# Kernel optimization log

Measured on AMD Instinct MI355X. Metric: run time of the kernel, lower is better.

The kernel has to match this reference:

```python
import jax, jax.numpy as jnp
import numpy as np

N_NODES = 100000
N_EDGES = 1600000
IN_DIM = 128
OUT_DIM = 64


def setup_inputs() -> dict:
    key = jax.random.key(0)
    k1, k2, k3, k4 = jax.random.split(key, 4)
    h = jax.random.normal(k1, (N_NODES, IN_DIM), dtype=jnp.float32)
    W = jax.random.normal(k2, (OUT_DIM, IN_DIM), dtype=jnp.float32) * (1.0 / np.sqrt(IN_DIM))
    a_w = jax.random.normal(k3, (1, 2 * OUT_DIM), dtype=jnp.float32) * (1.0 / np.sqrt(2 * OUT_DIM))
    edge_index = jax.random.randint(k4, (2, N_EDGES), 0, N_NODES, dtype=jnp.int64 if jax.config.jax_enable_x64 else jnp.int32)
    return {"h": h, "W": W, "a_w": a_w, "edge_index": edge_index}


def reference(h, W, a_w, edge_index):
    # Wh: [N, out_dim]  (Linear without bias: x @ W.T)
    Wh = h @ W.T
    src, dst = edge_index[0], edge_index[1]
    # per-edge concat [Wh[src], Wh[dst]] -> [E, 2*out_dim]
    e = jnp.concatenate([Wh[src], Wh[dst]], axis=-1)
    # attention logits: [E]
    alpha = jax.nn.leaky_relu(e @ a_w.T, negative_slope=0.2)[:, 0]
    # global-max-stabilized exp (matches the torch code exactly)
    alpha_exp = jnp.exp(alpha - jnp.max(alpha))
    # segment softmax denominator over destination nodes: [N]
    alpha_sum = jax.ops.segment_sum(alpha_exp, dst, num_segments=N_NODES)
    alpha_norm = alpha_exp / (alpha_sum[dst] + 1e-9)
    # weighted scatter-add aggregation: [N, out_dim]
    out = jax.ops.segment_sum(alpha_norm[:, None] * Wh[src], dst, num_segments=N_NODES)
    return (jax.nn.elu(out), alpha_norm)
```

## Files before the change

### kernel.cpp

```cpp
#include <hip/hip_runtime.h>
#include <math.h>

#define N_NODES 100000
#define N_EDGES 1600000
#define IN_DIM 128
#define OUT_DIM 64

#define BSHIFT 7
#define BSIZE  (1 << BSHIFT)
#define NB     ((N_NODES + BSIZE - 1) >> BSHIFT)
#define EDGES_PER_BLK 4096
#define NBLK   ((N_EDGES + EDGES_PER_BLK - 1) / EDGES_PER_BLK)
#define SCANA_LEN (NB * NBLK)
#define SCANA_ITEMS 1024
#define SCANA_NB ((SCANA_LEN + SCANA_ITEMS - 1) / SCANA_ITEMS)
#define REC_CAP 3072

typedef short short8 __attribute__((ext_vector_type(8)));
typedef float f32x4 __attribute__((ext_vector_type(4)));
typedef float f32x2 __attribute__((ext_vector_type(2)));

__device__ __forceinline__ unsigned short f2bf(float x) {
    unsigned int u = __float_as_uint(x);
    return (unsigned short)((u + 0x7FFFu + ((u >> 16) & 1u)) >> 16);
}
__device__ __forceinline__ short8 pack_bf16x8(float4 p, float4 q) {
    short8 r;
    r[0] = (short)f2bf(p.x); r[1] = (short)f2bf(p.y);
    r[2] = (short)f2bf(p.z); r[3] = (short)f2bf(p.w);
    r[4] = (short)f2bf(q.x); r[5] = (short)f2bf(q.y);
    r[6] = (short)f2bf(q.z); r[7] = (short)f2bf(q.w);
    return r;
}
__device__ __forceinline__ void pk_fma(f32x2& d, f32x2 a, f32x2 b) {
    asm("v_pk_fma_f32 %0, %1, %2, %0" : "+v"(d) : "v"(a), "v"(b));
}

__global__ __launch_bounds__(256) void k_histA(const int* __restrict__ dst,
                                               int* __restrict__ hist_t,
                                               const float* __restrict__ W,
                                               const float* __restrict__ a_w,
                                               float* __restrict__ w1,
                                               float* __restrict__ w2) {
    __shared__ int lhist[NB];
    const int tid = threadIdx.x;
    const int blk = blockIdx.x;
    if (blk == 0 && tid < IN_DIM) {
        float r1 = 0.f, r2 = 0.f;
        #pragma unroll 8
        for (int dd = 0; dd < OUT_DIM; ++dd) {
            float wv = W[dd * IN_DIM + tid];
            r1 = fmaf(a_w[dd], wv, r1);
            r2 = fmaf(a_w[OUT_DIM + dd], wv, r2);
        }
        w1[tid] = r1; w2[tid] = r2;
    }
    for (int i = tid; i < NB; i += 256) lhist[i] = 0;
    __syncthreads();
    const int e0 = blk * EDGES_PER_BLK;
    #pragma unroll
    for (int j = 0; j < 4; ++j) {
        int e = e0 + (j * 256 + tid) * 4;
        if (e >= N_EDGES) continue;
        int4 d4 = *(const int4*)(dst + e);
        atomicAdd(&lhist[d4.x >> BSHIFT], 1);
        atomicAdd(&lhist[d4.y >> BSHIFT], 1);
        atomicAdd(&lhist[d4.z >> BSHIFT], 1);
        atomicAdd(&lhist[d4.w >> BSHIFT], 1);
    }
    __syncthreads();
    for (int i = tid; i < NB; i += 256) hist_t[i * NBLK + blk] = lhist[i];
}

__global__ __launch_bounds__(256) void k_wh(const float* __restrict__ h,
                                            const float* __restrict__ W,
                                            const float* __restrict__ w1,
                                            const float* __restrict__ w2,
                                            unsigned short* __restrict__ Wh16,
                                            float* __restrict__ s1,
                                            float* __restrict__ s2) {
    const int tid = threadIdx.x;
    const int wv = tid >> 6;
    const int l  = tid & 63;
    const int g  = l >> 4;
    const int lm = l & 15;
    const int node0 = blockIdx.x * 64 + wv * 16;
    const int row = node0 + lm;
    const int rowc = (row < N_NODES) ? row : (N_NODES - 1);
    const float* hrow = h + (size_t)rowc * IN_DIM;

    short8 afrag[4];
    float sp1 = 0.f, sp2 = 0.f;
    #pragma unroll
    for (int kt = 0; kt < 4; ++kt) {
        const int k0 = kt * 32 + g * 8;
        float4 p = *(const float4*)(hrow + k0);
        float4 q = *(const float4*)(hrow + k0 + 4);
        float4 u1 = *(const float4*)(w1 + k0);
        float4 v1 = *(const float4*)(w1 + k0 + 4);
        float4 u2 = *(const float4*)(w2 + k0);
        float4 v2 = *(const float4*)(w2 + k0 + 4);
        sp1 += p.x*u1.x + p.y*u1.y + p.z*u1.z + p.w*u1.w
             + q.x*v1.x + q.y*v1.y + q.z*v1.z + q.w*v1.w;
        sp2 += p.x*u2.x + p.y*u2.y + p.z*u2.z + p.w*u2.w
             + q.x*v2.x + q.y*v2.y + q.z*v2.z + q.w*v2.w;
        afrag[kt] = pack_bf16x8(p, q);
    }
    sp1 += __shfl_xor(sp1, 16, 64); sp1 += __shfl_xor(sp1, 32, 64);
    sp2 += __shfl_xor(sp2, 16, 64); sp2 += __shfl_xor(sp2, 32, 64);
    if (l < 16 && row < N_NODES) { s1[row] = sp1; s2[row] = sp2; }

    f32x4 acc[4] = {f32x4{0,0,0,0}, f32x4{0,0,0,0}, f32x4{0,0,0,0}, f32x4{0,0,0,0}};
    #pragma unroll
    for (int nt = 0; nt < 4; ++nt) {
        #pragma unroll
        for (int kt = 0; kt < 4; ++kt) {
            const float* wr = W + (size_t)(nt * 16 + lm) * IN_DIM + kt * 32 + g * 8;
            float4 p = *(const float4*)wr;
            float4 q = *(const float4*)(wr + 4);
            short8 bfrag = pack_bf16x8(p, q);
            acc[nt] = __builtin_amdgcn_mfma_f32_16x16x32_bf16(afrag[kt], bfrag, acc[nt], 0, 0, 0);
        }
    }
    #pragma unroll
    for (int nt = 0; nt < 4; ++nt) {
        #pragma unroll
        for (int r = 0; r < 4; ++r) {
            int nodo = node0 + g * 4 + r;
            if (nodo < N_NODES)
                Wh16[(size_t)nodo * OUT_DIM + nt * 16 + lm] = f2bf(acc[nt][r]);
        }
    }
}

__global__ __launch_bounds__(256) void k_scanA_part(const int* __restrict__ in,
                                                    int* __restrict__ bsum) {
    __shared__ int wsum[4];
    const int tid = threadIdx.x;
    const int base = blockIdx.x * SCANA_ITEMS + tid * 4;
    int s = 0;
    #pragma unroll
    for (int j = 0; j < 4; ++j) {
        int i = base + j;
        if (i < SCANA_LEN) s += in[i];
    }
    #pragma unroll
    for (int off = 32; off > 0; off >>= 1) s += __shfl_xor(s, off, 64);
    if ((tid & 63) == 0) wsum[tid >> 6] = s;
    __syncthreads();
    if (tid == 0) bsum[blockIdx.x] = wsum[0] + wsum[1] + wsum[2] + wsum[3];
}

__global__ __launch_bounds__(512) void k_scanA_mid(int* __restrict__ bsum) {
    __shared__ int s[512];
    const int tid = threadIdx.x;
    s[tid] = (tid < SCANA_NB) ? bsum[tid] : 0;
    __syncthreads();
    #pragma unroll
    for (int off = 1; off < 512; off <<= 1) {
        int u = (tid >= off) ? s[tid - off] : 0;
        __syncthreads();
        s[tid] += u;
        __syncthreads();
    }
    if (tid < SCANA_NB) bsum[tid] = (tid > 0) ? s[tid - 1] : 0;
}

__global__ __launch_bounds__(256) void k_scanA_final(const int* __restrict__ in,
                                                     const int* __restrict__ bsum,
                                                     int* __restrict__ outscan) {
    __shared__ int wtot[4];
    const int tid = threadIdx.x;
    const int lane = tid & 63;
    const int wid = tid >> 6;
    const int base = blockIdx.x * SCANA_ITEMS + tid * 4;
    int c[4];
    #pragma unroll
    for (int j = 0; j < 4; ++j)
        c[j] = (base + j < SCANA_LEN) ? in[base + j] : 0;
    int tot = c[0] + c[1] + c[2] + c[3];
    int inc = tot;
    #pragma unroll
    for (int off = 1; off < 64; off <<= 1) {
        int u = __shfl_up(inc, off, 64);
        if (lane >= off) inc += u;
    }
    if (lane == 63) wtot[wid] = inc;
    __syncthreads();
    int wbase = 0;
    #pragma unroll
    for (int w = 0; w < 4; ++w) wbase += (w < wid) ? wtot[w] : 0;
    int run = bsum[blockIdx.x] + wbase + (inc - tot);
    #pragma unroll
    for (int j = 0; j < 4; ++j) {
        int i = base + j;
        if (i < SCANA_LEN) { outscan[i] = run; run += c[j]; }
    }
}

__global__ __launch_bounds__(256) void k_binA(const int* __restrict__ ei,
                                              const float* __restrict__ s1,
                                              const float* __restrict__ s2,
                                              const int* __restrict__ flat_scan,
                                              int2* __restrict__ brec,
                                              float* __restrict__ ae_orig) {
    __shared__ int lbase[NB];
    __shared__ int lcur[NB];
    const int tid = threadIdx.x;
    const int blk = blockIdx.x;
    for (int i = tid; i < NB; i += 256) { lbase[i] = flat_scan[i * NBLK + blk]; lcur[i] = 0; }
    __syncthreads();
    const int e0 = blk * EDGES_PER_BLK;
    #pragma unroll
    for (int j = 0; j < 4; ++j) {
        int e = e0 + (j * 256 + tid) * 4;
        if (e >= N_EDGES) continue;
        int4 s4 = *(const int4*)(ei + e);
        int4 d4 = *(const int4*)(ei + N_EDGES + e);
        float4 aev;
        #pragma unroll
        for (int q = 0; q < 4; ++q) {
            int src = ((const int*)&s4)[q];
            int dst = ((const int*)&d4)[q];
            float a = s1[src] + s2[dst];
            a = (a > 0.f) ? a : 0.2f * a;
            float ae = expf(a);
            ((float*)&aev)[q] = ae;
            int b = dst >> BSHIFT;
            int r = atomicAdd(&lcur[b], 1);
            brec[lbase[b] + r] = make_int2(src | ((dst & (BSIZE - 1)) << 17),
                                           __float_as_int(ae));
        }
        *(float4*)(ae_orig + e) = aev;
    }
}

__global__ __launch_bounds__(256) void k_fineagg(const int2* __restrict__ brec,
                                                 const int* __restrict__ flat_scan,
                                                 const unsigned short* __restrict__ Wh16,
                                                 float* __restrict__ out,
                                                 float* __restrict__ inv_tab) {
    __shared__ int2 lsorted[REC_CAP];
    __shared__ int lhist[BSIZE];
    __shared__ int lofs[BSIZE + 1];
    __shared__ int lcur[BSIZE];
    __shared__ float linv[BSIZE];
    const int tid = threadIdx.x;
    const int lane = tid & 63;
    const int wid = tid >> 6;
    const int b = blockIdx.x;
    const int base = flat_scan[b * NBLK];
    const int endp = (b + 1 < NB) ? flat_scan[(b + 1) * NBLK] : N_EDGES;
    const int cnt = endp - base;
    if (tid < BSIZE) lhist[tid] = 0;
    __syncthreads();
    for (int i = tid; i < cnt; i += 256)
        atomicAdd(&lhist[(unsigned)brec[base + i].x >> 17], 1);
    __syncthreads();
    if (wid == 0) {
        int c0 = lhist[2 * lane], c1 = lhist[2 * lane + 1];
        int s = c0 + c1;
        int inc = s;
        #pragma unroll
        for (int off = 1; off < 64; off <<= 1) {
            int u = __shfl_up(inc, off, 64);
            if (lane >= off) inc += u;
        }
        int ex = inc - s;
        lofs[2 * lane] = ex; lofs[2 * lane + 1] = ex + c0;
        lcur[2 * lane] = ex; lcur[2 * lane + 1] = ex + c0;
        if (lane == 63) lofs[BSIZE] = inc;
    }
    __syncthreads();
    for (int i = tid; i < cnt; i += 256) {
        int2 rec = brec[base + i];
        int dstl = (unsigned)rec.x >> 17;
        int pos = atomicAdd(&lcur[dstl], 1);
        lsorted[pos] = make_int2(rec.x & 0x1FFFF, rec.y);
    }
    __syncthreads();
    const int g = lane >> 3;
    const int o = lane & 7;
    const int dst0 = b << BSHIFT;
    for (int j = 0; j < 32; ++j) {
        const int bin = wid * 32 + j;
        const int node = dst0 + bin;
        if (node >= N_NODES) break;
        const int beg = lofs[bin];
        const int end2 = lofs[bin + 1];
        f32x2 acc2[4] = {f32x2{0,0}, f32x2{0,0}, f32x2{0,0}, f32x2{0,0}};
        float S = 0.f;
        int i = beg;
        for (; i + 16 <= end2; i += 16) {
            int2 pA = lsorted[i + g];
            int2 pB = lsorted[i + 8 + g];
            const int4 rA = *(const int4*)(Wh16 + ((size_t)pA.x << 6) + (o << 3));
            const int4 rB = *(const int4*)(Wh16 + ((size_t)pB.x << 6) + (o << 3));
            float aeA = __int_as_float(pA.y);
            float aeB = __int_as_float(pB.y);
            S += aeA + aeB;
            f32x2 a2A = {aeA, aeA}, a2B = {aeB, aeB};
            #pragma unroll
            for (int q = 0; q < 4; ++q) {
                int v = ((const int*)&rA)[q];
                f32x2 f = { __uint_as_float((unsigned)v << 16),
                            __uint_as_float((unsigned)v & 0xFFFF0000u) };
                pk_fma(acc2[q], f, a2A);
            }
            #pragma unroll
            for (int q = 0; q < 4; ++q) {
                int v = ((const int*)&rB)[q];
                f32x2 f = { __uint_as_float((unsigned)v << 16),
                            __uint_as_float((unsigned)v & 0xFFFF0000u) };
                pk_fma(acc2[q], f, a2B);
            }
        }
        for (; i < end2; i += 8) {
            int idx = i + g;
            int2 p = (idx < end2) ? lsorted[idx] : make_int2(0, 0);
            const int4 r = *(const int4*)(Wh16 + ((size_t)p.x << 6) + (o << 3));
            float ae = __int_as_float(p.y);
            S += ae;
            f32x2 a2 = {ae, ae};
            #pragma unroll
            for (int q = 0; q < 4; ++q) {
                int v = ((const int*)&r)[q];
                f32x2 f = { __uint_as_float((unsigned)v << 16),
                            __uint_as_float((unsigned)v & 0xFFFF0000u) };
                pk_fma(acc2[q], f, a2);
            }
        }
        #pragma unroll
        for (int m = 8; m <= 32; m <<= 1) {
            S += __shfl_xor(S, m, 64);
            #pragma unroll
            for (int q = 0; q < 4; ++q) {
                acc2[q].x += __shfl_xor(acc2[q].x, m, 64);
                acc2[q].y += __shfl_xor(acc2[q].y, m, 64);
            }
        }
        const float inv = 1.f / (S + 1e-9f);
        if (lane == 0) linv[bin] = inv;
        if (g == 0) {
            float e[8];
            #pragma unroll
            for (int q = 0; q < 4; ++q) {
                float x0 = acc2[q].x * inv;
                float x1 = acc2[q].y * inv;
                e[2*q]   = (x0 > 0.f) ? x0 : expf(x0) - 1.f;
                e[2*q+1] = (x1 > 0.f) ? x1 : expf(x1) - 1.f;
            }
            float* orow = out + (size_t)node * OUT_DIM + o * 8;
            *(float4*)orow = make_float4(e[0], e[1], e[2], e[3]);
            *(float4*)(orow + 4) = make_float4(e[4], e[5], e[6], e[7]);
        }
    }
    __syncthreads();
    if (tid < BSIZE) {
        int node = dst0 + tid;
        if (node < N_NODES) inv_tab[node] = linv[tid];
    }
}

__global__ __launch_bounds__(256) void k_norm(const int* __restrict__ dst_arr,
                                              const float* __restrict__ ae_orig,
                                              const float* __restrict__ inv_tab,
                                              float* __restrict__ alpha_norm) {
    int t = blockIdx.x * 256 + threadIdx.x;
    if (t >= N_EDGES / 4) return;
    int4 d4 = ((const int4*)dst_arr)[t];
    float4 a4 = ((const float4*)ae_orig)[t];
    float4 r;
    r.x = a4.x * inv_tab[d4.x];
    r.y = a4.y * inv_tab[d4.y];
    r.z = a4.z * inv_tab[d4.z];
    r.w = a4.w * inv_tab[d4.w];
    ((float4*)alpha_norm)[t] = r;
}

extern "C" void kernel_launch(void* const* d_in, const int* in_sizes, int n_in,
                              void* d_out, int out_size, void* d_ws, size_t ws_size,
                              hipStream_t stream) {
    const float* h   = (const float*)d_in[0];
    const float* W   = (const float*)d_in[1];
    const float* a_w = (const float*)d_in[2];
    const int*   ei  = (const int*)d_in[3];

    float* out        = (float*)d_out;
    float* alpha_norm = out + (size_t)N_NODES * OUT_DIM;

    char* ws = (char*)d_ws;
    int2* brec      = (int2*)ws;            ws += (size_t)N_EDGES * 8;
    unsigned short* Wh16 = (unsigned short*)ws;  ws += (size_t)N_NODES * OUT_DIM * 2;
    float* ae_orig  = (float*)ws;           ws += (size_t)N_EDGES * 4;
    float* s1       = (float*)ws;           ws += (size_t)N_NODES * 4;
    float* s2       = (float*)ws;           ws += (size_t)N_NODES * 4;
    int*   hist_t   = (int*)ws;             ws += (size_t)SCANA_LEN * 4;
    int*   flat_scan= (int*)ws;             ws += (size_t)SCANA_LEN * 4;
    int*   bsum     = (int*)ws;             ws += (size_t)SCANA_NB * 4;
    float* inv_tab  = (float*)ws;           ws += (size_t)N_NODES * 4;
    float* w1       = (float*)ws;           ws += (size_t)IN_DIM * 4;
    float* w2       = (float*)ws;           ws += (size_t)IN_DIM * 4;

    k_histA<<<NBLK, 256, 0, stream>>>(ei + N_EDGES, hist_t, W, a_w, w1, w2);
    k_wh<<<(N_NODES + 63) / 64, 256, 0, stream>>>(h, W, w1, w2, Wh16, s1, s2);
    k_scanA_part<<<SCANA_NB, 256, 0, stream>>>(hist_t, bsum);
    k_scanA_mid<<<1, 512, 0, stream>>>(bsum);
    k_scanA_final<<<SCANA_NB, 256, 0, stream>>>(hist_t, bsum, flat_scan);
    k_binA<<<NBLK, 256, 0, stream>>>(ei, s1, s2, flat_scan, brec, ae_orig);
    k_fineagg<<<NB, 256, 0, stream>>>(brec, flat_scan, Wh16, out, inv_tab);
    k_norm<<<(N_EDGES / 4 + 255) / 256, 256, 0, stream>>>(ei + N_EDGES, ae_orig,
                                                          inv_tab, alpha_norm);
}
```

Before: 170.7 us.

## Split fused fine-sort/aggregate into global sort kernel plus per-node aggregation kernel

Coarse bins grow from 128 to 512 nodes. The fused fine-sort+aggregate kernel is split in two. k_fine sorts records per destination into a global CSR array, writes per-node offsets, and computes softmax denominators with shared-memory float atomics. A separate k_agg launches one wavefront per node to gather and aggregate, so parallelism no longer depends on per-block LDS capacity or serial per-bin loops. The cost is an extra global round trip for the sorted records and one more kernel launch.

```diff
diff --git a/kernel.cpp b/kernel.cpp
--- a/kernel.cpp
+++ b/kernel.cpp
@@ -6,7 +6,7 @@
 #define IN_DIM 128
 #define OUT_DIM 64
 
-#define BSHIFT 7
+#define BSHIFT 9
 #define BSIZE  (1 << BSHIFT)
 #define NB     ((N_NODES + BSIZE - 1) >> BSHIFT)
 #define EDGES_PER_BLK 4096
@@ -14,7 +14,6 @@
 #define SCANA_LEN (NB * NBLK)
 #define SCANA_ITEMS 1024
 #define SCANA_NB ((SCANA_LEN + SCANA_ITEMS - 1) / SCANA_ITEMS)
-#define REC_CAP 3072
 
 typedef short short8 __attribute__((ext_vector_type(8)));
 typedef float f32x4 __attribute__((ext_vector_type(4)));
@@ -55,7 +54,7 @@
         }
         w1[tid] = r1; w2[tid] = r2;
     }
-    for (int i = tid; i < NB; i += 256) lhist[i] = 0;
+    if (tid < NB) lhist[tid] = 0;
     __syncthreads();
     const int e0 = blk * EDGES_PER_BLK;
     #pragma unroll
@@ -69,7 +68,7 @@
         atomicAdd(&lhist[d4.w >> BSHIFT], 1);
     }
     __syncthreads();
-    for (int i = tid; i < NB; i += 256) hist_t[i * NBLK + blk] = lhist[i];
+    if (tid < NB) hist_t[tid * NBLK + blk] = lhist[tid];
 }
 
 __global__ __launch_bounds__(256) void k_wh(const float* __restrict__ h,
@@ -151,13 +150,13 @@
     if (tid == 0) bsum[blockIdx.x] = wsum[0] + wsum[1] + wsum[2] + wsum[3];
 }
 
-__global__ __launch_bounds__(512) void k_scanA_mid(int* __restrict__ bsum) {
-    __shared__ int s[512];
+__global__ __launch_bounds__(128) void k_scanA_mid(int* __restrict__ bsum) {
+    __shared__ int s[128];
     const int tid = threadIdx.x;
     s[tid] = (tid < SCANA_NB) ? bsum[tid] : 0;
     __syncthreads();
     #pragma unroll
-    for (int off = 1; off < 512; off <<= 1) {
+    for (int off = 1; off < 128; off <<= 1) {
         int u = (tid >= off) ? s[tid - off] : 0;
         __syncthreads();
         s[tid] += u;
@@ -208,7 +207,7 @@
     __shared__ int lcur[NB];
     const int tid = threadIdx.x;
     const int blk = blockIdx.x;
-    for (int i = tid; i < NB; i += 256) { lbase[i] = flat_scan[i * NBLK + blk]; lcur[i] = 0; }
+    if (tid < NB) { lbase[tid] = flat_scan[tid * NBLK + blk]; lcur[tid] = 0; }
     __syncthreads();
     const int e0 = blk * EDGES_PER_BLK;
     #pragma unroll
@@ -235,16 +234,16 @@
     }
 }
 
-__global__ __launch_bounds__(256) void k_fineagg(const int2* __restrict__ brec,
-                                                 const int* __restrict__ flat_scan,
-                                                 const unsigned short* __restrict__ Wh16,
-                                                 float* __restrict__ out,
-                                                 float* __restrict__ inv_tab) {
-    __shared__ int2 lsorted[REC_CAP];
+__global__ __launch_bounds__(256) void k_fine(const int2* __restrict__ brec,
+                                              const int* __restrict__ flat_scan,
+                                              int* __restrict__ offsets,
+                                              int2* __restrict__ sa_sorted,
+                                              float* __restrict__ inv_tab) {
     __shared__ int lhist[BSIZE];
-    __shared__ int lofs[BSIZE + 1];
+    __shared__ int lofs[BSIZE];
     __shared__ int lcur[BSIZE];
-    __shared__ float linv[BSIZE];
+    __shared__ float lsum[BSIZE];
+    __shared__ int wsum[4];
     const int tid = threadIdx.x;
     const int lane = tid & 63;
     const int wid = tid >> 6;
@@ -252,113 +251,127 @@
     const int base = flat_scan[b * NBLK];
     const int endp = (b + 1 < NB) ? flat_scan[(b + 1) * NBLK] : N_EDGES;
     const int cnt = endp - base;
-    if (tid < BSIZE) lhist[tid] = 0;
+    lhist[tid] = 0; lhist[tid + 256] = 0;
+    lsum[tid] = 0.f; lsum[tid + 256] = 0.f;
     __syncthreads();
     for (int i = tid; i < cnt; i += 256)
         atomicAdd(&lhist[(unsigned)brec[base + i].x >> 17], 1);
     __syncthreads();
-    if (wid == 0) {
-        int c0 = lhist[2 * lane], c1 = lhist[2 * lane + 1];
-        int s = c0 + c1;
-        int inc = s;
-        #pragma unroll
-        for (int off = 1; off < 64; off <<= 1) {
-            int u = __shfl_up(inc, off, 64);
-            if (lane >= off) inc += u;
-        }
-        int ex = inc - s;
-        lofs[2 * lane] = ex; lofs[2 * lane + 1] = ex + c0;
-        lcur[2 * lane] = ex; lcur[2 * lane + 1] = ex + c0;
-        if (lane == 63) lofs[BSIZE] = inc;
-    }
-    __syncthreads();
+    int c0 = lhist[2 * tid], c1 = lhist[2 * tid + 1];
+    int s = c0 + c1;
+    int inc = s;
+    #pragma unroll
+    for (int off = 1; off < 64; off <<= 1) {
+        int u = __shfl_up(inc, off, 64);
+        if (lane >= off) inc += u;
+    }
+    if (lane == 63) wsum[wid] = inc;
+    __syncthreads();
+    int wb = 0;
+    #pragma unroll
+    for (int w = 0; w < 4; ++w) wb += (w < wid) ? wsum[w] : 0;
+    int ex = wb + inc - s;
+    lofs[2 * tid] = ex; lofs[2 * tid + 1] = ex + c0;
+    lcur[2 * tid] = ex; lcur[2 * tid + 1] = ex + c0;
+    __syncthreads();
+    const int dst0 = b << BSHIFT;
+    #pragma unroll
+    for (int j = 0; j < 2; ++j) {
+        int jj = tid + j * 256;
+        int node = dst0 + jj;
+        if (node < N_NODES) offsets[node] = base + lofs[jj];
+    }
+    if (b == NB - 1 && tid == 0) offsets[N_NODES] = N_EDGES;
     for (int i = tid; i < cnt; i += 256) {
         int2 rec = brec[base + i];
         int dstl = (unsigned)rec.x >> 17;
-        int pos = atomicAdd(&lcur[dstl], 1);
-        lsorted[pos] = make_int2(rec.x & 0x1FFFF, rec.y);
-    }
-    __syncthreads();
-    const int g = lane >> 3;
-    const int o = lane & 7;
-    const int dst0 = b << BSHIFT;
-    for (int j = 0; j < 32; ++j) {
-        const int bin = wid * 32 + j;
-        const int node = dst0 + bin;
-        if (node >= N_NODES) break;
-        const int beg = lofs[bin];
-        const int end2 = lofs[bin + 1];
-        f32x2 acc2[4] = {f32x2{0,0}, f32x2{0,0}, f32x2{0,0}, f32x2{0,0}};
-        float S = 0.f;
-        int i = beg;
-        for (; i + 16 <= end2; i += 16) {
-            int2 pA = lsorted[i + g];
-            int2 pB = lsorted[i + 8 + g];
-            const int4 rA = *(const int4*)(Wh16 + ((size_t)pA.x << 6) + (o << 3));
-            const int4 rB = *(const int4*)(Wh16 + ((size_t)pB.x << 6) + (o << 3));
-            float aeA = __int_as_float(pA.y);
-            float aeB = __int_as_float(pB.y);
-            S += aeA + aeB;
-            f32x2 a2A = {aeA, aeA}, a2B = {aeB, aeB};
-            #pragma unroll
-            for (int q = 0; q < 4; ++q) {
-                int v = ((const int*)&rA)[q];
-                f32x2 f = { __uint_as_float((unsigned)v << 16),
-                            __uint_as_float((unsigned)v & 0xFFFF0000u) };
-                pk_fma(acc2[q], f, a2A);
-            }
-            #pragma unroll
-            for (int q = 0; q < 4; ++q) {
-                int v = ((const int*)&rB)[q];
-                f32x2 f = { __uint_as_float((unsigned)v << 16),
-                            __uint_as_float((unsigned)v & 0xFFFF0000u) };
-                pk_fma(acc2[q], f, a2B);
-            }
-        }
-        for (; i < end2; i += 8) {
-            int idx = i + g;
-            int2 p = (idx < end2) ? lsorted[idx] : make_int2(0, 0);
-            const int4 r = *(const int4*)(Wh16 + ((size_t)p.x << 6) + (o << 3));
-            float ae = __int_as_float(p.y);
-            S += ae;
-            f32x2 a2 = {ae, ae};
-            #pragma unroll
-            for (int q = 0; q < 4; ++q) {
-                int v = ((const int*)&r)[q];
-                f32x2 f = { __uint_as_float((unsigned)v << 16),
-                            __uint_as_float((unsigned)v & 0xFFFF0000u) };
-                pk_fma(acc2[q], f, a2);
-            }
-        }
-        #pragma unroll
-        for (int m = 8; m <= 32; m <<= 1) {
-            S += __shfl_xor(S, m, 64);
-            #pragma unroll
-            for (int q = 0; q < 4; ++q) {
-                acc2[q].x += __shfl_xor(acc2[q].x, m, 64);
-                acc2[q].y += __shfl_xor(acc2[q].y, m, 64);
-            }
-        }
-        const float inv = 1.f / (S + 1e-9f);
-        if (lane == 0) linv[bin] = inv;
-        if (g == 0) {
-            float e[8];
-            #pragma unroll
-            for (int q = 0; q < 4; ++q) {
-                float x0 = acc2[q].x * inv;
-                float x1 = acc2[q].y * inv;
-                e[2*q]   = (x0 > 0.f) ? x0 : expf(x0) - 1.f;
-                e[2*q+1] = (x1 > 0.f) ? x1 : expf(x1) - 1.f;
-            }
-            float* orow = out + (size_t)node * OUT_DIM + o * 8;
-            *(float4*)orow = make_float4(e[0], e[1], e[2], e[3]);
-            *(float4*)(orow + 4) = make_float4(e[4], e[5], e[6], e[7]);
-        }
-    }
-    __syncthreads();
-    if (tid < BSIZE) {
-        int node = dst0 + tid;
-        if (node < N_NODES) inv_tab[node] = linv[tid];
+        float ae = __int_as_float(rec.y);
+        int pos = base + atomicAdd(&lcur[dstl], 1);
+        sa_sorted[pos] = make_int2(rec.x & 0x1FFFF, rec.y);
+        atomicAdd(&lsum[dstl], ae);
+    }
+    __syncthreads();
+    #pragma unroll
+    for (int j = 0; j < 2; ++j) {
+        int jj = tid + j * 256;
+        int node = dst0 + jj;
+        if (node < N_NODES) inv_tab[node] = 1.f / (lsum[jj] + 1e-9f);
+    }
+}
+
+__global__ __launch_bounds__(256) void k_agg(const int2* __restrict__ sa_sorted,
+                                             const int* __restrict__ offsets,
+                                             const unsigned short* __restrict__ Wh16,
+                                             const float* __restrict__ inv_tab,
+                                             float* __restrict__ out) {
+    const int gid = blockIdx.x * 256 + threadIdx.x;
+    const int node = gid >> 6;
+    const int l = gid & 63;
+    if (node >= N_NODES) return;
+    const int g = l >> 3;
+    const int o = l & 7;
+    const int beg = offsets[node];
+    const int end = offsets[node + 1];
+    f32x2 acc2[4] = {f32x2{0,0}, f32x2{0,0}, f32x2{0,0}, f32x2{0,0}};
+    int i = beg;
+    for (; i + 16 <= end; i += 16) {
+        int2 pA = sa_sorted[i + g];
+        int2 pB = sa_sorted[i + 8 + g];
+        const int4 rA = *(const int4*)(Wh16 + ((size_t)pA.x << 6) + (o << 3));
+        const int4 rB = *(const int4*)(Wh16 + ((size_t)pB.x << 6) + (o << 3));
+        float aeA = __int_as_float(pA.y);
+        float aeB = __int_as_float(pB.y);
+        f32x2 a2A = {aeA, aeA}, a2B = {aeB, aeB};
+        #pragma unroll
+        for (int q = 0; q < 4; ++q) {
+            int v = ((const int*)&rA)[q];
+            f32x2 f = { __uint_as_float((unsigned)v << 16),
+                        __uint_as_float((unsigned)v & 0xFFFF0000u) };
+            pk_fma(acc2[q], f, a2A);
+        }
+        #pragma unroll
+        for (int q = 0; q < 4; ++q) {
+            int v = ((const int*)&rB)[q];
+            f32x2 f = { __uint_as_float((unsigned)v << 16),
+                        __uint_as_float((unsigned)v & 0xFFFF0000u) };
+            pk_fma(acc2[q], f, a2B);
+        }
+    }
+    for (; i < end; i += 8) {
+        int idx = i + g;
+        int2 p = (idx < end) ? sa_sorted[idx] : make_int2(0, 0);
+        const int4 r = *(const int4*)(Wh16 + ((size_t)p.x << 6) + (o << 3));
+        float ae = __int_as_float(p.y);
+        f32x2 a2 = {ae, ae};
+        #pragma unroll
+        for (int q = 0; q < 4; ++q) {
+            int v = ((const int*)&r)[q];
+            f32x2 f = { __uint_as_float((unsigned)v << 16),
+                        __uint_as_float((unsigned)v & 0xFFFF0000u) };
+            pk_fma(acc2[q], f, a2);
+        }
+    }
+    #pragma unroll
+    for (int m = 8; m <= 32; m <<= 1) {
+        #pragma unroll
+        for (int q = 0; q < 4; ++q) {
+            acc2[q].x += __shfl_xor(acc2[q].x, m, 64);
+            acc2[q].y += __shfl_xor(acc2[q].y, m, 64);
+        }
+    }
+    if (g == 0) {
+        const float inv = inv_tab[node];
+        float e[8];
+        #pragma unroll
+        for (int q = 0; q < 4; ++q) {
+            float x0 = acc2[q].x * inv;
+            float x1 = acc2[q].y * inv;
+            e[2*q]   = (x0 > 0.f) ? x0 : expf(x0) - 1.f;
+            e[2*q+1] = (x1 > 0.f) ? x1 : expf(x1) - 1.f;
+        }
+        float* orow = out + (size_t)node * OUT_DIM + o * 8;
+        *(float4*)orow = make_float4(e[0], e[1], e[2], e[3]);
+        *(float4*)(orow + 4) = make_float4(e[4], e[5], e[6], e[7]);
     }
 }
 
@@ -391,6 +404,7 @@
 
     char* ws = (char*)d_ws;
     int2* brec      = (int2*)ws;            ws += (size_t)N_EDGES * 8;
+    int2* sa_sorted = (int2*)ws;            ws += (size_t)N_EDGES * 8;
     unsigned short* Wh16 = (unsigned short*)ws;  ws += (size_t)N_NODES * OUT_DIM * 2;
     float* ae_orig  = (float*)ws;           ws += (size_t)N_EDGES * 4;
     float* s1       = (float*)ws;           ws += (size_t)N_NODES * 4;
@@ -398,6 +412,7 @@
     int*   hist_t   = (int*)ws;             ws += (size_t)SCANA_LEN * 4;
     int*   flat_scan= (int*)ws;             ws += (size_t)SCANA_LEN * 4;
     int*   bsum     = (int*)ws;             ws += (size_t)SCANA_NB * 4;
+    int*   offsets  = (int*)ws;             ws += (size_t)(N_NODES + 1) * 4;
     float* inv_tab  = (float*)ws;           ws += (size_t)N_NODES * 4;
     float* w1       = (float*)ws;           ws += (size_t)IN_DIM * 4;
     float* w2       = (float*)ws;           ws += (size_t)IN_DIM * 4;
@@ -405,10 +420,12 @@
     k_histA<<<NBLK, 256, 0, stream>>>(ei + N_EDGES, hist_t, W, a_w, w1, w2);
     k_wh<<<(N_NODES + 63) / 64, 256, 0, stream>>>(h, W, w1, w2, Wh16, s1, s2);
     k_scanA_part<<<SCANA_NB, 256, 0, stream>>>(hist_t, bsum);
-    k_scanA_mid<<<1, 512, 0, stream>>>(bsum);
+    k_scanA_mid<<<1, 128, 0, stream>>>(bsum);
     k_scanA_final<<<SCANA_NB, 256, 0, stream>>>(hist_t, bsum, flat_scan);
     k_binA<<<NBLK, 256, 0, stream>>>(ei, s1, s2, flat_scan, brec, ae_orig);
-    k_fineagg<<<NB, 256, 0, stream>>>(brec, flat_scan, Wh16, out, inv_tab);
+    k_fine<<<NB, 256, 0, stream>>>(brec, flat_scan, offsets, sa_sorted, inv_tab);
+    k_agg<<<(N_NODES * 64 + 255) / 256, 256, 0, stream>>>(sa_sorted, offsets, Wh16,
+                                                          inv_tab, out);
     k_norm<<<(N_EDGES / 4 + 255) / 256, 256, 0, stream>>>(ei + N_EDGES, ae_orig,
                                                           inv_tab, alpha_norm);
 }
```

Measured after the change: 165.2 us. -3.2%, faster.
